# Optimization experiments

Measured on AMD Instinct MI355X. Metric: run time of the kernel, lower is better.

Reference implementation:

```python
import jax, jax.numpy as jnp
import numpy as np

B, N, D, C, H, W = 4, 900, 256, 256, 200, 200
HEADS, LVLS, PTS, K = 8, 1, 4, 10


def setup_inputs() -> dict:
    key = jax.random.key(0)
    ks = jax.random.split(key, 16)
    s = 0.02
    return {
        "query_embed": jax.random.normal(ks[0], (B, N, D), jnp.float32),
        "ctrl_points": jax.random.uniform(ks[1], (B, N, 4, 2), jnp.float32, -50.0, 50.0),
        "bev_features": jax.random.normal(ks[2], (B, C, H, W), jnp.float32),
        "spatial_shapes": jnp.array([[H, W]], dtype=jnp.int32),
        "pc_range": jnp.array([-51.2, -51.2, -5.0, 51.2, 51.2, 3.0], jnp.float32),
        "Wq": s * jax.random.normal(ks[3], (D, D)), "bq": jnp.zeros((D,)),
        "Wv": s * jax.random.normal(ks[4], (C, D)), "bv": jnp.zeros((D,)),
        "Woff": s * jax.random.normal(ks[5], (D, HEADS * LVLS * PTS * 2)), "boff": jnp.zeros((HEADS * LVLS * PTS * 2,)),
        "Wattn": s * jax.random.normal(ks[6], (D, HEADS * LVLS * PTS)), "battn": jnp.zeros((HEADS * LVLS * PTS,)),
        "Wmo": s * jax.random.normal(ks[7], (D, D)), "bmo": jnp.zeros((D,)),
        "Wo": s * jax.random.normal(ks[8], (D, D)), "bo": jnp.zeros((D,)),
    }


def _forward(query_embed, ctrl_points, bev_features, spatial_shapes, pc_range,
             Wq, bq, Wv, bv, Woff, boff, Wattn, battn, Wmo, bmo, Wo, bo):
    b, n, d = query_embed.shape
    _, c, h, w = bev_features.shape
    hd = d // HEADS

    # --- cubic Bezier interpolation: (B,N,4,2) -> (B,N,K,2) dense points ---
    t = jnp.linspace(0.0, 1.0, K, dtype=query_embed.dtype)
    basis = jnp.stack([(1 - t) ** 3, 3 * (1 - t) ** 2 * t, 3 * (1 - t) * t ** 2, t ** 3], axis=-1)  # (K,4)
    dense = jnp.einsum('kc,bncd->bnkd', basis, ctrl_points)
    # --- normalize to [0,1] by pc_range, clamp to [0.01,0.99] ---
    nx = (dense[..., 0] - pc_range[0]) / (pc_range[3] - pc_range[0])
    ny = (dense[..., 1] - pc_range[1]) / (pc_range[4] - pc_range[1])
    ref = jnp.clip(jnp.stack([nx, ny], axis=-1), 0.01, 0.99)  # (B,N,K,2)

    # --- projections ---
    q = query_embed @ Wq + bq                                       # (B,N,D) (identity for residual)
    v = bev_features.reshape(b, c, h * w).transpose(0, 2, 1) @ Wv + bv  # (B,HW,D)
    v = v.reshape(b, h * w, HEADS, hd)

    off = (q @ Woff + boff).reshape(b, n, HEADS, LVLS, PTS, 2)
    aw = jax.nn.softmax((q @ Wattn + battn).reshape(b, n, HEADS, LVLS * PTS), axis=-1)
    aw = aw.reshape(b, n, HEADS, PTS)  # LVLS == 1

    # offset normalizer = (W, H) per level
    normalizer = jnp.stack([spatial_shapes[..., 1], spatial_shapes[..., 0]], axis=-1).astype(q.dtype)  # (L,2)
    # sampling locations: broadcast K bezier points against heads/points offsets
    loc = ref[:, :, None, :, None, :] + off / normalizer[None, None, None, :, None, :]  # (B,N,HEADS,K,PTS,2)

    # --- bilinear sampling, align_corners=False, zero padding ---
    gx = loc[..., 0] * w - 0.5
    gy = loc[..., 1] * h - 0.5
    x0 = jnp.floor(gx)
    y0 = jnp.floor(gy)
    wx = gx - x0
    wy = gy - y0
    x0i = x0.astype(jnp.int32)
    y0i = y0.astype(jnp.int32)

    vflat = v.transpose(0, 2, 1, 3).reshape(b * HEADS, h * w, hd)  # (B*HEADS, HW, hd)

    def flat(a):  # (B,N,HEADS,K,PTS) -> (B*HEADS, N*K*PTS)
        return a.transpose(0, 2, 1, 3, 4).reshape(b * HEADS, n * K * PTS)

    acc = jnp.zeros((b * HEADS, n * K * PTS, hd), dtype=q.dtype)
    for dx, dy in ((0, 0), (1, 0), (0, 1), (1, 1)):
        ix = flat(x0i) + dx
        iy = flat(y0i) + dy
        wxx = flat(wx) if dx else (1.0 - flat(wx))
        wyy = flat(wy) if dy else (1.0 - flat(wy))
        valid = (ix >= 0) & (ix < w) & (iy >= 0) & (iy < h)
        idx = jnp.clip(iy, 0, h - 1) * w + jnp.clip(ix, 0, w - 1)
        corner = jnp.take_along_axis(vflat, idx[..., None], axis=1)  # (B*HEADS, Npts, hd)
        acc = acc + corner * (wxx * wyy * valid.astype(q.dtype))[..., None]

    sampled = acc.reshape(b, HEADS, n, K, PTS, hd)
    # weighted sum over (K, PTS); attention weights shared across the K bezier points
    out = jnp.einsum('bhnkpd,bnhp->bnhd', sampled, aw).reshape(b, n, d)
    out = out @ Wmo + bmo + q   # mmcv MSDeformAttn output_proj + residual (identity = query)
    out = out @ Wo + bo         # outer output_proj
    return out


def reference(query_embed, ctrl_points, bev_features, spatial_shapes, pc_range,
              Wq, bq, Wv, bv, Woff, boff, Wattn, battn, Wmo, bmo, Wo, bo):
    return _forward(query_embed, ctrl_points, bev_features, spatial_shapes, pc_range,
                    Wq, bq, Wv, bv, Woff, boff, Wattn, battn, Wmo, bmo, Wo, bo)
```

## Files before the change

### kernel.cpp

```cpp
#include <hip/hip_runtime.h>
#include <hip/hip_bf16.h>
#include <math.h>


typedef unsigned short u16;
typedef unsigned int u32;
typedef short bf16x8 __attribute__((ext_vector_type(8)));
typedef float f32x4 __attribute__((ext_vector_type(4)));

__device__ __forceinline__ float bflo(u32 w) {
  union { u32 i; float f; } c; c.i = w << 16; return c.f;
}
__device__ __forceinline__ float bfhi(u32 w) {
  union { u32 i; float f; } c; c.i = w & 0xffff0000u; return c.f;
}
__device__ __forceinline__ u16 f2bf(float f) {
  union { float f; u32 i; } c; c.f = f;
  u32 u = c.i;
  return (u16)((u + 0x7FFFu + ((u >> 16) & 1u)) >> 16);
}
__device__ __forceinline__ int imin(int a, int b) { return a < b ? a : b; }
__device__ __forceinline__ int imax(int a, int b) { return a > b ? a : b; }

__device__ __forceinline__ void glds16(const u16* g, u16* l) {
  __builtin_amdgcn_global_load_lds(
      (__attribute__((address_space(1))) const void*)g,
      (__attribute__((address_space(3))) void*)l, 16, 0, 0);
}

__global__ __launch_bounds__(256) void prep_weights(
    const float* __restrict__ Wq, const float* __restrict__ Wv,
    const float* __restrict__ Woff, const float* __restrict__ Wattn,
    const float* __restrict__ Wmo, const float* __restrict__ Wo,
    const float* __restrict__ bq, const float* __restrict__ boff,
    const float* __restrict__ battn, const float* __restrict__ bmo,
    const float* __restrict__ bo, const float* __restrict__ query,
    u16* __restrict__ bqoaT, u16* __restrict__ wvT, u16* __restrict__ woCat,
    float* __restrict__ bcat, float* __restrict__ bprime,
    u16* __restrict__ qin)
{
  const int idx = blockIdx.x * 256 + threadIdx.x;
  {
    int i = idx * 4;
    float4 v = *(const float4*)(query + i);
    uint2 st;
    st.x = (u32)f2bf(v.x) | ((u32)f2bf(v.y) << 16);
    st.y = (u32)f2bf(v.z) | ((u32)f2bf(v.w) << 16);
    *(uint2*)(qin + i) = st;
  }
  if (idx < 65536) {
    int r = idx >> 8, c = idx & 255;
    bqoaT[idx] = f2bf(Wq[c * 256 + r]);
    wvT[idx]   = f2bf(Wv[c * 256 + r]);
  }
  if (idx < 24576) {
    int n = idx >> 8, k = idx & 255;
    const float* wq = Wq + k * 256;
    float s = 0.f;
    if (n < 64) {
      const float* wo = Woff + n;
#pragma unroll 4
      for (int c = 0; c < 256; c += 4) {
        float4 a = *(const float4*)(wq + c);
        s += a.x * wo[(c + 0) * 64] + a.y * wo[(c + 1) * 64] +
             a.z * wo[(c + 2) * 64] + a.w * wo[(c + 3) * 64];
      }
    } else {
      const float* wa = Wattn + (n - 64);
#pragma unroll 4
      for (int c = 0; c < 256; c += 4) {
        float4 a = *(const float4*)(wq + c);
        s += a.x * wa[(c + 0) * 32] + a.y * wa[(c + 1) * 32] +
             a.z * wa[(c + 2) * 32] + a.w * wa[(c + 3) * 32];
      }
    }
    bqoaT[65536 + idx] = f2bf(s);
  }
  if (idx < 131072) {
    int n = idx >> 9, k = idx & 511;
    float s;
    if (k >= 256) {
      s = Wo[(size_t)(k - 256) * 256 + n];
    } else {
      const float* wm = Wmo + k * 256;
      const float* wo = Wo + n;
      s = 0.f;
#pragma unroll 4
      for (int c = 0; c < 256; c += 4) {
        float4 a = *(const float4*)(wm + c);
        s += a.x * wo[(c + 0) * 256] + a.y * wo[(c + 1) * 256] +
             a.z * wo[(c + 2) * 256] + a.w * wo[(c + 3) * 256];
      }
    }
    woCat[idx] = f2bf(s);
  }
  if (idx >= 131072 && idx < 131328) {
    int n = idx - 131072;
    const float* wo = Wo + n;
    float s = bo[n];
    for (int c = 0; c < 256; ++c) s += bmo[c] * wo[c * 256];
    bprime[n] = s;
  }
  if (idx >= 131328 && idx < 131680) {
    int n = idx - 131328;
    if (n < 256) {
      bcat[n] = bq[n];
    } else {
      int j = n - 256;
      float s;
      if (j < 64) {
        const float* wo = Woff + j;
        s = boff[j];
        for (int c = 0; c < 256; ++c) s += bq[c] * wo[c * 64];
      } else {
        const float* wa = Wattn + (j - 64);
        s = battn[j - 64];
        for (int c = 0; c < 256; ++c) s += bq[c] * wa[c * 32];
      }
      bcat[n] = s;
    }
  }
}

enum { GM_F32 = 0, GM_SPLIT = 1 };

template <int MODE>
__global__ __launch_bounds__(256) void gemm_bt(
    const u16* __restrict__ A, const u16* __restrict__ Bt,
    const float* __restrict__ bias,
    u16* __restrict__ outb, float* __restrict__ outf,
    int M, int N, int K, int lda, int ldo)
{
  __shared__ __align__(16) u16 lA[128 * 32];
  __shared__ __align__(16) u16 lB[128 * 32];
  const int tid = threadIdx.x;
  const int wv = tid >> 6, lane = tid & 63;
  const int m0 = blockIdx.y * 128;
  const int n0 = blockIdx.x * 128;

  const int crow = lane >> 2;
  const int ckoff = (lane & 3) * 8;
  const int a1 = imin(m0 + wv * 16 + crow, M - 1);
  const int a2 = imin(m0 + (wv + 4) * 16 + crow, M - 1);
  const int b1 = imin(n0 + wv * 16 + crow, N - 1);
  const int b2 = imin(n0 + (wv + 4) * 16 + crow, N - 1);
  const u16* gA1 = A + (size_t)a1 * lda + ckoff;
  const u16* gA2 = A + (size_t)a2 * lda + ckoff;
  const u16* gB1 = Bt + (size_t)b1 * K + ckoff;
  const u16* gB2 = Bt + (size_t)b2 * K + ckoff;
  u16* lA1 = lA + wv * 512;  u16* lA2 = lA + (wv + 4) * 512;
  u16* lB1 = lB + wv * 512;  u16* lB2 = lB + (wv + 4) * 512;

  const int fm = (wv & 1) * 64, fn = (wv >> 1) * 64;
  const int fr = lane & 15, fk = (lane >> 4) * 8;

  f32x4 acc[4][4];
#pragma unroll
  for (int i = 0; i < 4; ++i)
#pragma unroll
    for (int j = 0; j < 4; ++j) acc[i][j] = (f32x4){0.f, 0.f, 0.f, 0.f};

  for (int k0 = 0; k0 < K; k0 += 32) {
    glds16(gA1 + k0, lA1);
    glds16(gA2 + k0, lA2);
    glds16(gB1 + k0, lB1);
    glds16(gB2 + k0, lB2);
    __syncthreads();
    bf16x8 af[4], bfv[4];
#pragma unroll
    for (int i = 0; i < 4; ++i)
      af[i] = *(const bf16x8*)&lA[(fm + i * 16 + fr) * 32 + fk];
#pragma unroll
    for (int j = 0; j < 4; ++j)
      bfv[j] = *(const bf16x8*)&lB[(fn + j * 16 + fr) * 32 + fk];
    __syncthreads();
#pragma unroll
    for (int i = 0; i < 4; ++i)
#pragma unroll
      for (int j = 0; j < 4; ++j)
        acc[i][j] = __builtin_amdgcn_mfma_f32_16x16x32_bf16(af[i], bfv[j], acc[i][j], 0, 0, 0);
  }

  const int quad = lane >> 4;
#pragma unroll
  for (int j = 0; j < 4; ++j) {
    const int n = n0 + fn + j * 16 + fr;
    const bool nok = (n < N);
    const float bcol = bias[nok ? n : 0];
#pragma unroll
    for (int i = 0; i < 4; ++i) {
      const int mb = m0 + fm + i * 16 + quad * 4;
#pragma unroll
      for (int r = 0; r < 4; ++r) {
        const int m = mb + r;
        if (m < M && nok) {
          float x = acc[i][j][r] + bcol;
          if (MODE == GM_F32) {
            outf[(size_t)m * ldo + n] = x;
          } else {
            if (n < 256) outb[(size_t)m * 512 + n] = f2bf(x);
            else outf[(size_t)m * 96 + (n - 256)] = x;
          }
        }
      }
    }
  }
}

__global__ __launch_bounds__(256) void gemm_v(
    const u16* __restrict__ A,
    const float* __restrict__ bev,
    const float* __restrict__ bias,
    u16* __restrict__ outb)
{
  __shared__ __align__(16) u16 lA[128 * 32];
  __shared__ __align__(16) u16 lB[128 * 32];
  const int tid = threadIdx.x;
  const int wv = tid >> 6, lane = tid & 63;
  const int m0 = blockIdx.x * 128;
  const int n0 = blockIdx.y * 128;
  const int z = blockIdx.z;

  const int crow = lane >> 2, ckoff = (lane & 3) * 8;
  const u16* gA1 = A + (size_t)(m0 + wv * 16 + crow) * 256 + ckoff;
  const u16* gA2 = A + (size_t)(m0 + (wv + 4) * 16 + crow) * 256 + ckoff;
  u16* lA1 = lA + wv * 512;  u16* lA2 = lA + (wv + 4) * 512;

  const int kp = tid >> 4, nb = tid & 15;
  const int cb = imin(n0 + nb * 8, 40000 - 8);
  const float* src = bev + ((size_t)z * 256 + 2 * kp) * 40000 + cb;
  const int wslot = (((kp >> 2) ^ (nb & 3)) << 2) + (kp & 3);
  u32* lBw = (u32*)lB;
  const int wrow = nb * 8;

  const int fm = (wv & 1) * 64, fn = (wv >> 1) * 64;
  const int fr = lane & 15, fk = (lane >> 4) * 8;

  f32x4 acc[4][4];
#pragma unroll
  for (int i = 0; i < 4; ++i)
#pragma unroll
    for (int j = 0; j < 4; ++j) acc[i][j] = (f32x4){0.f, 0.f, 0.f, 0.f};

  float4 r0 = *(const float4*)(src);
  float4 r1 = *(const float4*)(src + 4);
  float4 r2 = *(const float4*)(src + 40000);
  float4 r3 = *(const float4*)(src + 40004);

  for (int k0 = 0; k0 < 256; k0 += 32) {
    glds16(gA1 + k0, lA1);
    glds16(gA2 + k0, lA2);
#define CVW(nn, a, b)                                                        \
    { u32 pk;                                                                \
      asm("v_cvt_pk_bf16_f32 %0, %1, %2" : "=v"(pk) : "v"(a), "v"(b));       \
      lBw[(wrow + (nn)) * 16 + wslot] = pk; }
    CVW(0, r0.x, r2.x) CVW(1, r0.y, r2.y) CVW(2, r0.z, r2.z) CVW(3, r0.w, r2.w)
    CVW(4, r1.x, r3.x) CVW(5, r1.y, r3.y) CVW(6, r1.z, r3.z) CVW(7, r1.w, r3.w)
#undef CVW
    if (k0 < 224) {
      const float* s2 = src + (size_t)(k0 + 32) * 40000;
      r0 = *(const float4*)(s2);
      r1 = *(const float4*)(s2 + 4);
      r2 = *(const float4*)(s2 + 40000);
      r3 = *(const float4*)(s2 + 40004);
    }
    __syncthreads();
    bf16x8 af[4], bfv[4];
#pragma unroll
    for (int i = 0; i < 4; ++i)
      af[i] = *(const bf16x8*)&lA[(fm + i * 16 + fr) * 32 + fk];
#pragma unroll
    for (int j = 0; j < 4; ++j) {
      const int n = fn + j * 16 + fr;
      const int pc = (((lane >> 4) ^ ((n >> 3) & 3)) << 3);
      bfv[j] = *(const bf16x8*)&lB[n * 32 + pc];
    }
    __syncthreads();
#pragma unroll
    for (int i = 0; i < 4; ++i)
#pragma unroll
      for (int j = 0; j < 4; ++j)
        acc[i][j] = __builtin_amdgcn_mfma_f32_16x16x32_bf16(af[i], bfv[j], acc[i][j], 0, 0, 0);
  }

  const int quad = lane >> 4;
#pragma unroll
  for (int j = 0; j < 4; ++j) {
    const int n = n0 + fn + j * 16 + fr;
    if (n < 40000) {
#pragma unroll
      for (int i = 0; i < 4; ++i) {
        const int mb = m0 + fm + i * 16 + quad * 4;
        u16 u0 = f2bf(acc[i][j][0] + bias[mb + 0]);
        u16 u1 = f2bf(acc[i][j][1] + bias[mb + 1]);
        u16 u2 = f2bf(acc[i][j][2] + bias[mb + 2]);
        u16 u3 = f2bf(acc[i][j][3] + bias[mb + 3]);
        size_t off = (size_t)z * (8ull * 40000 * 32) +
                     (size_t)(mb >> 5) * (40000 * 32) + (size_t)n * 32 + (mb & 31);
        uint2 st; st.x = (u32)u0 | ((u32)u1 << 16); st.y = (u32)u2 | ((u32)u3 << 16);
        *(uint2*)(outb + off) = st;
      }
    }
  }
}

__global__ __launch_bounds__(256) void sampler(
    const float* __restrict__ ctrl,
    const float* __restrict__ pc,
    const float* __restrict__ oa_,
    const u16* __restrict__ v,
    u16* __restrict__ attn_out)
{
  __shared__ int   sX0[4][40], sY0[4][40];
  __shared__ float sWx[4][40], sWy[4][40], sAw[4][40];
  const int w = threadIdx.x >> 6, lane = threadIdx.x & 63;
  const int bh = blockIdx.x & 31;
  const int n = (blockIdx.x >> 5) * 4 + w;
  const int h = bh & 7, b = bh >> 3;
  const int row = b * 900 + n;

  if (lane < 40) {
    const int k = lane >> 2, p = lane & 3;
    const float t = (float)k * (1.0f / 9.0f), u = 1.f - t;
    const float c0 = u * u * u, c1 = 3.f * u * u * t, c2 = 3.f * u * t * t, c3 = t * t * t;
    const float* cp = ctrl + (size_t)row * 8;
    float cx = c0 * cp[0] + c1 * cp[2] + c2 * cp[4] + c3 * cp[6];
    float cy = c0 * cp[1] + c1 * cp[3] + c2 * cp[5] + c3 * cp[7];
    float nx = (cx - pc[0]) / (pc[3] - pc[0]);
    float ny = (cy - pc[1]) / (pc[4] - pc[1]);
    nx = fminf(fmaxf(nx, 0.01f), 0.99f);
    ny = fminf(fmaxf(ny, 0.01f), 0.99f);
    const float* oa = oa_ + (size_t)row * 96;
    float ox = oa[h * 8 + p * 2 + 0], oy = oa[h * 8 + p * 2 + 1];
    float l0 = oa[64 + h * 4 + 0], l1 = oa[64 + h * 4 + 1];
    float l2 = oa[64 + h * 4 + 2], l3 = oa[64 + h * 4 + 3];
    float mx = fmaxf(fmaxf(l0, l1), fmaxf(l2, l3));
    float e0 = __expf(l0 - mx), e1 = __expf(l1 - mx), e2 = __expf(l2 - mx), e3 = __expf(l3 - mx);
    float lp = (p == 0) ? l0 : (p == 1) ? l1 : (p == 2) ? l2 : l3;
    float aw = __expf(lp - mx) / (e0 + e1 + e2 + e3);
    float gx = (nx + ox * (1.f / 200.f)) * 200.f - 0.5f;
    float gy = (ny + oy * (1.f / 200.f)) * 200.f - 0.5f;
    float x0 = floorf(gx), y0 = floorf(gy);
    sX0[w][lane] = (int)x0; sY0[w][lane] = (int)y0;
    sWx[w][lane] = gx - x0; sWy[w][lane] = gy - y0; sAw[w][lane] = aw;
  }
  __syncthreads();

  const int sg = lane >> 3;
  const int ch0 = (lane & 7) * 4;
  const u16* vb = v + ((size_t)(b * 8 + h)) * (40000 * 32) + ch0;
  float a0 = 0.f, a1 = 0.f, a2 = 0.f, a3 = 0.f;
#pragma unroll
  for (int p = 0; p < 5; ++p) {
    const int s = p * 8 + sg;
    const int x0 = sX0[w][s], y0 = sY0[w][s];
    const float wx = sWx[w][s], wy = sWy[w][s], aw = sAw[w][s];
    const int x1 = x0 + 1, y1 = y0 + 1;
    const int cx0 = imin(imax(x0, 0), 199), cx1 = imin(imax(x1, 0), 199);
    const int cy0 = imin(imax(y0, 0), 199), cy1 = imin(imax(y1, 0), 199);
    const bool vx0 = (u32)x0 < 200u, vx1 = (u32)x1 < 200u;
    const bool vy0 = (u32)y0 < 200u, vy1 = (u32)y1 < 200u;
    const float w00 = (vx0 && vy0) ? aw * (1.f - wx) * (1.f - wy) : 0.f;
    const float w10 = (vx1 && vy0) ? aw * wx * (1.f - wy) : 0.f;
    const float w01 = (vx0 && vy1) ? aw * (1.f - wx) * wy : 0.f;
    const float w11 = (vx1 && vy1) ? aw * wx * wy : 0.f;
    uint2 d00 = *(const uint2*)(vb + (size_t)(cy0 * 200 + cx0) * 32);
    uint2 d10 = *(const uint2*)(vb + (size_t)(cy0 * 200 + cx1) * 32);
    uint2 d01 = *(const uint2*)(vb + (size_t)(cy1 * 200 + cx0) * 32);
    uint2 d11 = *(const uint2*)(vb + (size_t)(cy1 * 200 + cx1) * 32);
    a0 += w00 * bflo(d00.x) + w10 * bflo(d10.x) + w01 * bflo(d01.x) + w11 * bflo(d11.x);
    a1 += w00 * bfhi(d00.x) + w10 * bfhi(d10.x) + w01 * bfhi(d01.x) + w11 * bfhi(d11.x);
    a2 += w00 * bflo(d00.y) + w10 * bflo(d10.y) + w01 * bflo(d01.y) + w11 * bflo(d11.y);
    a3 += w00 * bfhi(d00.y) + w10 * bfhi(d10.y) + w01 * bfhi(d01.y) + w11 * bfhi(d11.y);
  }
#pragma unroll
  for (int off = 8; off < 64; off <<= 1) {
    a0 += __shfl_xor(a0, off);
    a1 += __shfl_xor(a1, off);
    a2 += __shfl_xor(a2, off);
    a3 += __shfl_xor(a3, off);
  }
  if (lane < 8) {
    uint2 st;
    st.x = (u32)f2bf(a0) | ((u32)f2bf(a1) << 16);
    st.y = (u32)f2bf(a2) | ((u32)f2bf(a3) << 16);
    *(uint2*)(attn_out + (size_t)row * 512 + h * 32 + ch0) = st;
  }
}

extern "C" void kernel_launch(void* const* d_in, const int* in_sizes, int n_in,
                              void* d_out, int out_size, void* d_ws, size_t ws_size,
                              hipStream_t stream)
{
  const float* query = (const float*)d_in[0];
  const float* ctrl  = (const float*)d_in[1];
  const float* bev   = (const float*)d_in[2];
  const float* pc    = (const float*)d_in[4];
  const float* Wq    = (const float*)d_in[5];  const float* bq    = (const float*)d_in[6];
  const float* Wv    = (const float*)d_in[7];  const float* bv    = (const float*)d_in[8];
  const float* Woff  = (const float*)d_in[9];  const float* boff  = (const float*)d_in[10];
  const float* Wattn = (const float*)d_in[11]; const float* battn = (const float*)d_in[12];
  const float* Wmo   = (const float*)d_in[13]; const float* bmo   = (const float*)d_in[14];
  const float* Wo    = (const float*)d_in[15]; const float* bo    = (const float*)d_in[16];

  char* ws = (char*)d_ws;
  size_t off = 0;
  auto alloc = [&](size_t bytes) -> void* {
    void* p = ws + off; off += (bytes + 255) & ~(size_t)255; return p;
  };
  u16*  v     = (u16*)alloc(4ull * 8 * 40000 * 32 * 2);
  u16*  qin   = (u16*)alloc(3600ull * 256 * 2);
  u16*  wvT   = (u16*)alloc(65536 * 2);
  u16*  bqoaT = (u16*)alloc(352 * 256 * 2);
  u16*  woCat = (u16*)alloc(256 * 512 * 2);
  float* bcat = (float*)alloc(352 * 4);
  float* bprime = (float*)alloc(256 * 4);
  float* oaf  = (float*)alloc(3600ull * 96 * 4);
  u16*  qcat  = (u16*)alloc(3600ull * 512 * 2);
  (void)ws_size; (void)in_sizes; (void)n_in; (void)out_size;

  prep_weights<<<900, 256, 0, stream>>>(Wq, Wv, Woff, Wattn, Wmo, Wo,
                                        bq, boff, battn, bmo, bo, query,
                                        bqoaT, wvT, woCat, bcat, bprime, qin);
  gemm_v<<<dim3(2, 313, 4), 256, 0, stream>>>(wvT, bev, bv, v);
  gemm_bt<GM_SPLIT><<<dim3(3, 29), 256, 0, stream>>>(
      qin, bqoaT, bcat, qcat + 256, oaf, 3600, 352, 256, 256, 0);
  sampler<<<7200, 256, 0, stream>>>(ctrl, pc, oaf, v, qcat);
  gemm_bt<GM_F32><<<dim3(2, 29), 256, 0, stream>>>(
      qcat, woCat, bprime, nullptr, (float*)d_out, 3600, 256, 512, 512, 256);
}
```

Measured before the change: 377.7 us.

## Preload full A tile and double-buffer B in value-projection GEMM

Measured after the change: 376.2 us. About the same (-0.4%).

```diff
diff --git a/kernel.cpp b/kernel.cpp
--- a/kernel.cpp
+++ b/kernel.cpp
@@ -207,14 +207,40 @@
   }
 }
 
-__global__ __launch_bounds__(256) void gemm_v(
+#define LOADB(S, R0, R1, R2, R3)                                   \
+  { const float* s2_ = src + (size_t)((S) * 32) * 40000;           \
+    R0 = *(const float4*)(s2_);                                    \
+    R1 = *(const float4*)(s2_ + 4);                                \
+    R2 = *(const float4*)(s2_ + 40000);                            \
+    R3 = *(const float4*)(s2_ + 40004); }
+
+#define CVW8(BUF, R0, R1, R2, R3)                                            \
+  { u32* lbw_ = (u32*)(BUF); u32 pk_;                                        \
+    asm("v_cvt_pk_bf16_f32 %0, %1, %2" : "=v"(pk_) : "v"(R0.x), "v"(R2.x)); \
+    lbw_[(wrow + 0) * 16 + wslot] = pk_;                                     \
+    asm("v_cvt_pk_bf16_f32 %0, %1, %2" : "=v"(pk_) : "v"(R0.y), "v"(R2.y)); \
+    lbw_[(wrow + 1) * 16 + wslot] = pk_;                                     \
+    asm("v_cvt_pk_bf16_f32 %0, %1, %2" : "=v"(pk_) : "v"(R0.z), "v"(R2.z)); \
+    lbw_[(wrow + 2) * 16 + wslot] = pk_;                                     \
+    asm("v_cvt_pk_bf16_f32 %0, %1, %2" : "=v"(pk_) : "v"(R0.w), "v"(R2.w)); \
+    lbw_[(wrow + 3) * 16 + wslot] = pk_;                                     \
+    asm("v_cvt_pk_bf16_f32 %0, %1, %2" : "=v"(pk_) : "v"(R1.x), "v"(R3.x)); \
+    lbw_[(wrow + 4) * 16 + wslot] = pk_;                                     \
+    asm("v_cvt_pk_bf16_f32 %0, %1, %2" : "=v"(pk_) : "v"(R1.y), "v"(R3.y)); \
+    lbw_[(wrow + 5) * 16 + wslot] = pk_;                                     \
+    asm("v_cvt_pk_bf16_f32 %0, %1, %2" : "=v"(pk_) : "v"(R1.z), "v"(R3.z)); \
+    lbw_[(wrow + 6) * 16 + wslot] = pk_;                                     \
+    asm("v_cvt_pk_bf16_f32 %0, %1, %2" : "=v"(pk_) : "v"(R1.w), "v"(R3.w)); \
+    lbw_[(wrow + 7) * 16 + wslot] = pk_; }
+
+__global__ __launch_bounds__(256, 2) void gemm_v(
     const u16* __restrict__ A,
     const float* __restrict__ bev,
     const float* __restrict__ bias,
     u16* __restrict__ outb)
 {
-  __shared__ __align__(16) u16 lA[128 * 32];
-  __shared__ __align__(16) u16 lB[128 * 32];
+  __shared__ __align__(16) u16 lA[8 * 128 * 32];
+  __shared__ __align__(16) u16 lB[2][128 * 32];
   const int tid = threadIdx.x;
   const int wv = tid >> 6, lane = tid & 63;
   const int m0 = blockIdx.x * 128;
@@ -224,13 +250,13 @@
   const int crow = lane >> 2, ckoff = (lane & 3) * 8;
   const u16* gA1 = A + (size_t)(m0 + wv * 16 + crow) * 256 + ckoff;
   const u16* gA2 = A + (size_t)(m0 + (wv + 4) * 16 + crow) * 256 + ckoff;
-  u16* lA1 = lA + wv * 512;  u16* lA2 = lA + (wv + 4) * 512;
+  u16* lA1 = lA + wv * 512;
+  u16* lA2 = lA + (wv + 4) * 512;
 
   const int kp = tid >> 4, nb = tid & 15;
   const int cb = imin(n0 + nb * 8, 40000 - 8);
   const float* src = bev + ((size_t)z * 256 + 2 * kp) * 40000 + cb;
   const int wslot = (((kp >> 2) ^ (nb & 3)) << 2) + (kp & 3);
-  u32* lBw = (u32*)lB;
   const int wrow = nb * 8;
 
   const int fm = (wv & 1) * 64, fn = (wv >> 1) * 64;
@@ -242,45 +268,56 @@
 #pragma unroll
     for (int j = 0; j < 4; ++j) acc[i][j] = (f32x4){0.f, 0.f, 0.f, 0.f};
 
-  float4 r0 = *(const float4*)(src);
-  float4 r1 = *(const float4*)(src + 4);
-  float4 r2 = *(const float4*)(src + 40000);
-  float4 r3 = *(const float4*)(src + 40004);
-
-  for (int k0 = 0; k0 < 256; k0 += 32) {
-    glds16(gA1 + k0, lA1);
-    glds16(gA2 + k0, lA2);
-#define CVW(nn, a, b)                                                        \
-    { u32 pk;                                                                \
-      asm("v_cvt_pk_bf16_f32 %0, %1, %2" : "=v"(pk) : "v"(a), "v"(b));       \
-      lBw[(wrow + (nn)) * 16 + wslot] = pk; }
-    CVW(0, r0.x, r2.x) CVW(1, r0.y, r2.y) CVW(2, r0.z, r2.z) CVW(3, r0.w, r2.w)
-    CVW(4, r1.x, r3.x) CVW(5, r1.y, r3.y) CVW(6, r1.z, r3.z) CVW(7, r1.w, r3.w)
-#undef CVW
-    if (k0 < 224) {
-      const float* s2 = src + (size_t)(k0 + 32) * 40000;
-      r0 = *(const float4*)(s2);
-      r1 = *(const float4*)(s2 + 4);
-      r2 = *(const float4*)(s2 + 40000);
-      r3 = *(const float4*)(s2 + 40004);
-    }
-    __syncthreads();
+  float4 ra0, ra1, ra2, ra3, rb0, rb1, rb2, rb3;
+
+  LOADB(0, ra0, ra1, ra2, ra3);
+#pragma unroll
+  for (int s = 0; s < 8; ++s) {
+    glds16(gA1 + s * 32, lA1 + s * 4096);
+    glds16(gA2 + s * 32, lA2 + s * 4096);
+  }
+  asm volatile("" ::: "memory");
+  CVW8(lB[0], ra0, ra1, ra2, ra3);
+  asm volatile("" ::: "memory");
+  LOADB(1, rb0, rb1, rb2, rb3);
+  __builtin_amdgcn_sched_barrier(0);
+  asm volatile("s_waitcnt vmcnt(4) lgkmcnt(0)" ::: "memory");
+  __builtin_amdgcn_sched_barrier(0);
+  __builtin_amdgcn_s_barrier();
+  __builtin_amdgcn_sched_barrier(0);
+
+#pragma unroll
+  for (int t = 0; t < 8; ++t) {
     bf16x8 af[4], bfv[4];
 #pragma unroll
     for (int i = 0; i < 4; ++i)
-      af[i] = *(const bf16x8*)&lA[(fm + i * 16 + fr) * 32 + fk];
+      af[i] = *(const bf16x8*)&lA[t * 4096 + (fm + i * 16 + fr) * 32 + fk];
 #pragma unroll
     for (int j = 0; j < 4; ++j) {
       const int n = fn + j * 16 + fr;
       const int pc = (((lane >> 4) ^ ((n >> 3) & 3)) << 3);
-      bfv[j] = *(const bf16x8*)&lB[n * 32 + pc];
-    }
-    __syncthreads();
+      bfv[j] = *(const bf16x8*)&lB[t & 1][n * 32 + pc];
+    }
+    if (t < 7) {
+      if ((t & 1) == 0) { CVW8(lB[1], rb0, rb1, rb2, rb3); }
+      else              { CVW8(lB[0], ra0, ra1, ra2, ra3); }
+    }
+    if (t < 6) {
+      if ((t & 1) == 0) { LOADB(t + 2, ra0, ra1, ra2, ra3); }
+      else              { LOADB(t + 2, rb0, rb1, rb2, rb3); }
+    }
 #pragma unroll
     for (int i = 0; i < 4; ++i)
 #pragma unroll
       for (int j = 0; j < 4; ++j)
         acc[i][j] = __builtin_amdgcn_mfma_f32_16x16x32_bf16(af[i], bfv[j], acc[i][j], 0, 0, 0);
+    if (t < 7) {
+      __builtin_amdgcn_sched_barrier(0);
+      asm volatile("s_waitcnt lgkmcnt(0)" ::: "memory");
+      __builtin_amdgcn_sched_barrier(0);
+      __builtin_amdgcn_s_barrier();
+      __builtin_amdgcn_sched_barrier(0);
+    }
   }
 
   const int quad = lane >> 4;
```
